# Optimization experiments

Hardware: AMD Instinct MI355X
Metric: run time of the kernel (lower is better)

The kernel has to match this reference:

```python
import jax, jax.numpy as jnp
import numpy as np

PNS = (1, 2, 3, 4, 6, 8, 12, 16)
N_E, E_DIM = 8192, 256
BETA = 0.25
ALPHA = 0.5  # abs(quant_resi)
B, HW = 64, 16


def _area_mat(out_n, in_n):
    # torch adaptive_avg_pool1d matrix (F.interpolate mode='area')
    M = np.zeros((out_n, in_n), np.float32)
    for i in range(out_n):
        s = (i * in_n) // out_n
        e = -((-(i + 1) * in_n) // out_n)  # ceil((i+1)*in_n/out_n)
        M[i, s:e] = 1.0 / (e - s)
    return M


def _cubic_w(t):
    a = -0.75  # torch bicubic coefficient
    t = abs(t)
    if t <= 1.0:
        return (a + 2) * t ** 3 - (a + 3) * t ** 2 + 1.0
    if t < 2.0:
        return a * t ** 3 - 5 * a * t ** 2 + 8 * a * t - 4 * a
    return 0.0


def _bicubic_mat(out_n, in_n):
    # torch F.interpolate mode='bicubic', align_corners=False, border-replicate taps
    M = np.zeros((out_n, in_n), np.float32)
    scale = in_n / out_n
    for i in range(out_n):
        x = (i + 0.5) * scale - 0.5
        f = int(np.floor(x))
        for k in range(-1, 3):
            idx = min(max(f + k, 0), in_n - 1)
            M[i, idx] += _cubic_w(x - (f + k))
    return M


def setup_inputs() -> dict:
    key = jax.random.key(0)
    k1, k2, k3 = jax.random.split(key, 3)
    z = jax.random.normal(k1, (B, E_DIM, HW, HW), jnp.float32)
    embedding = jax.random.normal(k2, (N_E, E_DIM), jnp.float32)
    conv_w = jax.random.normal(k3, (len(PNS), E_DIM, E_DIM, 3, 3), jnp.float32) * 0.02
    conv_b = jnp.zeros((len(PNS), E_DIM), jnp.float32)
    return {"z": z, "embedding": embedding, "conv_w": conv_w, "conv_b": conv_b}


def reference(z, embedding, conv_w, conv_b):
    Bz, C, H, W = z.shape
    S = len(PNS)
    z_rest = z
    z_hat = jnp.zeros_like(z)
    total_loss = jnp.zeros((), z.dtype)
    counts = jnp.zeros((N_E,), z.dtype)
    e_sq = jnp.sum(embedding ** 2, axis=1)  # [n_e]
    for si, pn in enumerate(PNS):
        if si != S - 1:
            A = jnp.asarray(_area_mat(pn, H))
            zd = jnp.einsum('ph,qw,bchw->bpqc', A, A, z_rest)  # [B,pn,pn,C]
        else:
            zd = jnp.transpose(z_rest, (0, 2, 3, 1))
        zf = zd.reshape(-1, C)  # [N,C]
        dist = jnp.sum(zf ** 2, axis=1, keepdims=True) + e_sq - 2.0 * (zf @ embedding.T)
        idx = jnp.argmin(dist, axis=1)  # [N]
        zk = embedding[idx].reshape(zd.shape)  # [B,pn,pn,C]
        zk = jnp.transpose(zk, (0, 3, 1, 2))  # [B,C,pn,pn]
        if si != S - 1:
            U = jnp.asarray(_bicubic_mat(H, pn))
            zu = jnp.einsum('hp,wq,bcpq->bchw', U, U, zk)
        else:
            zu = zk
        y = jax.lax.conv_general_dilated(
            zu, conv_w[si], (1, 1), 'SAME',
            dimension_numbers=('NCHW', 'OIHW', 'NCHW')) + conv_b[si][None, :, None, None]
        res = zu * (1.0 - ALPHA) + y * ALPHA
        z_hat = z_hat + res
        z_rest = z_rest - res
        counts = counts.at[idx].add(jnp.asarray(1.0, z.dtype))
        total_loss = total_loss + BETA * jnp.mean((jax.lax.stop_gradient(z_hat) - z) ** 2)
    mean_vq_loss = total_loss / S
    z_hat_out = z + jax.lax.stop_gradient(z_hat - z)
    return z_hat_out, mean_vq_loss, counts
```

## Files before the change

kernel.cpp:

```cpp
#include <hip/hip_runtime.h>
#include <math.h>

#define NB 64
#define NC 256
#define NHW 16
#define NE 8192
#define NUMEL 4194304
#define LOSS_OFF 4194304
#define CNT_OFF  4194305

typedef __bf16 bf16x8 __attribute__((ext_vector_type(8)));
typedef float  f32x4  __attribute__((ext_vector_type(4)));

#define GLOAD_LDS(gptr, lptr) \
  __builtin_amdgcn_global_load_lds( \
      (const __attribute__((address_space(1))) unsigned int*)(gptr), \
      (__attribute__((address_space(3))) unsigned int*)(lptr), 16, 0, 0)

__device__ __forceinline__ float cubicw(float t) {
  t = fabsf(t);
  if (t <= 1.0f) return (1.25f * t - 2.25f) * t * t + 1.0f;
  if (t < 2.0f)  return ((-0.75f * t + 3.75f) * t - 6.0f) * t + 3.0f;
  return 0.0f;
}

__device__ __forceinline__ short f2bf(float x) {
  union { float f; unsigned int u; } v; v.f = x;
  unsigned int r = v.u + 0x7fffu + ((v.u >> 16) & 1u);
  return (short)(r >> 16);
}
__device__ __forceinline__ float bf2f(short h) {
  union { float f; unsigned int u; } v;
  v.u = ((unsigned int)(unsigned short)h) << 16;
  return v.f;
}

__global__ void k_zero(float* a, int na) {
  int i = blockIdx.x * 256 + threadIdx.x;
  if (i < na) a[i] = 0.0f;
}

__global__ void k_tr_in(const float* __restrict__ z, float* __restrict__ zrest) {
  int n = blockIdx.x, c = threadIdx.x;
  int b = n >> 8, hw = n & 255;
  zrest[(size_t)n * 256 + c] = z[((size_t)(b * 256 + c)) * 256 + hw];
}

__global__ void k_prep_emb2(const float* __restrict__ emb, short* __restrict__ B2,
                            float* __restrict__ esq) {
  int j = blockIdx.x, t = threadIdx.x;
  float v = emb[(size_t)j * 256 + t];
  short hi = f2bf(v);
  short lo = f2bf(v - bf2f(hi));
  B2[(size_t)j * 768 + t]       = hi;
  B2[(size_t)j * 768 + 256 + t] = hi;
  B2[(size_t)j * 768 + 512 + t] = lo;
  __shared__ float red[256];
  red[t] = v * v;
  __syncthreads();
  for (int s = 128; s > 0; s >>= 1) { if (t < s) red[t] += red[t + s]; __syncthreads(); }
  if (t == 0) esq[j] = red[0];
}

__global__ void k_prep_wb(const float* __restrict__ w, short* __restrict__ wB2) {
  int m = blockIdx.x * 256 + threadIdx.x;
  if (m >= 8 * 9 * 65536) return;
  int i = m & 255, o = (m >> 8) & 255;
  int r = m >> 16;
  int si = r / 9, tap = r % 9;
  float v = w[(((size_t)si * 256 + o) * 256 + i) * 9 + tap];
  short hi = f2bf(v);
  short lo = f2bf(v - bf2f(hi));
  size_t dst = ((size_t)r * 256 + o) * 768;
  wB2[dst + i]       = hi;
  wB2[dst + 256 + i] = hi;
  wB2[dst + 512 + i] = lo;
}

__global__ void k_down_a2(const float* __restrict__ zrest, short* __restrict__ A2, int pn) {
  int pq = blockIdx.x, b = blockIdx.y, c = threadIdx.x;
  int p = pq / pn, q = pq % pn;
  int sp = (p * 16) / pn, ep = ((p + 1) * 16 + pn - 1) / pn;
  int sq = (q * 16) / pn, eq = ((q + 1) * 16 + pn - 1) / pn;
  float s = 0.0f;
  for (int h = sp; h < ep; h++)
    for (int w = sq; w < eq; w++)
      s += zrest[((size_t)((b * 16 + h) * 16 + w)) * 256 + c];
  float x = s / (float)((ep - sp) * (eq - sq));
  int n = (b * pn + p) * pn + q;
  short hi = f2bf(x);
  short lo = f2bf(x - bf2f(hi));
  A2[(size_t)n * 768 + c]       = hi;
  A2[(size_t)n * 768 + 256 + c] = lo;
  A2[(size_t)n * 768 + 512 + c] = hi;
}

__global__ void k_split_a2(const float* __restrict__ zrest, short* __restrict__ A2) {
  int n = blockIdx.x, c = threadIdx.x;
  float x = zrest[(size_t)n * 256 + c];
  short hi = f2bf(x);
  short lo = f2bf(x - bf2f(hi));
  A2[(size_t)n * 768 + c]       = hi;
  A2[(size_t)n * 768 + 256 + c] = lo;
  A2[(size_t)n * 768 + 512 + c] = hi;
}

__global__ __launch_bounds__(512, 2) void k_dist_mfma(
    const short* __restrict__ A2, const short* __restrict__ B2,
    const float* __restrict__ esq, float* __restrict__ pd, int* __restrict__ pi,
    int N) {
  __shared__ short As[4][8192];
  __shared__ short Bs[4][8192];
  int t = threadIdx.x, ln = t & 63, wv = t >> 6;
  int wr = wv >> 2, wc = wv & 3;
  int n0 = blockIdx.x * 256;
  int jb0 = blockIdx.y * 256;
  int lc = ln & 15, lq = ln >> 4;

  const short* gA[2]; const short* gB[2]; int ldst[2];
#pragma unroll
  for (int i = 0; i < 2; i++) {
    int C = i * 512 + wv * 64 + ln;
    int L = C >> 3, c5s = C & 7;
    int c5g = c5s ^ (L & 7);
    int rowg = (L << 1) | (c5g >> 2), ccg = c5g & 3;
    gA[i] = A2 + (size_t)(n0 + rowg) * 768 + ccg * 8;
    gB[i] = B2 + (size_t)(jb0 + rowg) * 768 + ccg * 8;
    ldst[i] = (i * 512 + wv * 64) * 8;
  }
  int offA[2][4], offB[4];
#pragma unroll
  for (int rt = 0; rt < 4; rt++) {
#pragma unroll
    for (int h = 0; h < 2; h++) {
      int row = wr * 128 + h * 64 + rt * 16 + lc;
      int L = row >> 1;
      int swc = (((row & 1) << 2) + lq) ^ (L & 7);
      offA[h][rt] = L * 64 + swc * 8;
    }
    int rowb = wc * 64 + rt * 16 + lc;
    int Lb = rowb >> 1;
    int swb = (((rowb & 1) << 2) + lq) ^ (Lb & 7);
    offB[rt] = Lb * 64 + swb * 8;
  }

  f32x4 acc[8][4];
#pragma unroll
  for (int at = 0; at < 8; at++)
#pragma unroll
    for (int ac = 0; ac < 4; ac++) acc[at][ac] = (f32x4)(0.0f);

#define DSTAGE_A(tile_, bsel_)                                        \
  {                                                                   \
    _Pragma("unroll")                                                 \
    for (int i = 0; i < 2; i++)                                       \
      GLOAD_LDS(gA[i] + (tile_) * 32, &As[(bsel_)][ldst[i]]);         \
  }
#define DSTAGE_B(tile_, bsel_)                                        \
  {                                                                   \
    _Pragma("unroll")                                                 \
    for (int i = 0; i < 2; i++)                                       \
      GLOAD_LDS(gB[i] + (tile_) * 32, &Bs[(bsel_)][ldst[i]]);         \
  }

  DSTAGE_A(0, 0); DSTAGE_B(0, 0);
  DSTAGE_A(1, 1); DSTAGE_B(1, 1);
  DSTAGE_A(2, 2); DSTAGE_B(2, 2);
  asm volatile("s_waitcnt vmcnt(8)" ::: "memory");
  __builtin_amdgcn_s_barrier();

#pragma unroll
  for (int kt = 0; kt < 24; kt++) {
    const int bsel = kt & 3;
    const short* aBase = &As[bsel][0];
    const short* bBase = &Bs[bsel][0];
    if (kt < 21) DSTAGE_A(kt + 3, (kt + 3) & 3);
    bf16x8 fa0[4], fb[4];
#pragma unroll
    for (int rt = 0; rt < 4; rt++)
      fa0[rt] = *(const bf16x8*)(aBase + offA[0][rt]);
#pragma unroll
    for (int ct = 0; ct < 4; ct++)
      fb[ct] = *(const bf16x8*)(bBase + offB[ct]);
    __builtin_amdgcn_s_barrier();
    asm volatile("s_waitcnt lgkmcnt(0)" ::: "memory");
    __builtin_amdgcn_s_setprio(1);
#pragma unroll
    for (int rt = 0; rt < 4; rt++)
#pragma unroll
      for (int ct = 0; ct < 4; ct++)
        acc[rt][ct] = __builtin_amdgcn_mfma_f32_16x16x32_bf16(
            fa0[rt], fb[ct], acc[rt][ct], 0, 0, 0);
    __builtin_amdgcn_s_setprio(0);
    __builtin_amdgcn_s_barrier();
    if (kt < 21) DSTAGE_B(kt + 3, (kt + 3) & 3);
    bf16x8 fa1[4];
#pragma unroll
    for (int rt = 0; rt < 4; rt++)
      fa1[rt] = *(const bf16x8*)(aBase + offA[1][rt]);
    __builtin_amdgcn_s_barrier();
    asm volatile("s_waitcnt lgkmcnt(0)" ::: "memory");
    __builtin_amdgcn_s_setprio(1);
#pragma unroll
    for (int rt = 0; rt < 4; rt++)
#pragma unroll
      for (int ct = 0; ct < 4; ct++)
        acc[4 + rt][ct] = __builtin_amdgcn_mfma_f32_16x16x32_bf16(
            fa1[rt], fb[ct], acc[4 + rt][ct], 0, 0, 0);
    __builtin_amdgcn_s_setprio(0);
    if (kt < 23) {
      if (kt < 21)       { asm volatile("s_waitcnt vmcnt(8)" ::: "memory"); }
      else if (kt == 21) { asm volatile("s_waitcnt vmcnt(4)" ::: "memory"); }
      else               { asm volatile("s_waitcnt vmcnt(0)" ::: "memory"); }
      __builtin_amdgcn_s_barrier();
    }
  }
#undef DSTAGE_A
#undef DSTAGE_B

  float* sbd = (float*)(&As[0][0]);
  int*   sbi = (int*)((char*)(&As[0][0]) + 4096);

#pragma unroll
  for (int at = 0; at < 8; at++) {
    float bst[4]; int bix[4];
#pragma unroll
    for (int r = 0; r < 4; r++) { bst[r] = 3.4e38f; bix[r] = 0; }
#pragma unroll
    for (int ac = 0; ac < 4; ac++) {
      int j = jb0 + wc * 64 + ac * 16 + lc;
      float es = esq[j];
#pragma unroll
      for (int r = 0; r < 4; r++) {
        float d = es - 2.0f * acc[at][ac][r];
        if (d < bst[r]) { bst[r] = d; bix[r] = j; }
      }
    }
#pragma unroll
    for (int r = 0; r < 4; r++) {
      float bd = bst[r]; int bi = bix[r];
#pragma unroll
      for (int off = 1; off < 16; off <<= 1) {
        float od = __shfl_xor(bd, off, 64);
        int   oi = __shfl_xor(bi, off, 64);
        if (od < bd || (od == bd && oi < bi)) { bd = od; bi = oi; }
      }
      if (lc == 0) {
        int rl = wr * 128 + at * 16 + lq * 4 + r;
        sbd[wc * 256 + rl] = bd;
        sbi[wc * 256 + rl] = bi;
      }
    }
  }
  __syncthreads();
  if (t < 256) {
    float b0 = sbd[t]; int i0 = sbi[t];
#pragma unroll
    for (int w = 1; w < 4; w++) {
      float b1 = sbd[w * 256 + t]; int i1 = sbi[w * 256 + t];
      if (b1 < b0 || (b1 == b0 && i1 < i0)) { b0 = b1; i0 = i1; }
    }
    int n = n0 + t;
    if (n < N) {
      pd[(size_t)n * 32 + blockIdx.y] = b0;
      pi[(size_t)n * 32 + blockIdx.y] = i0;
    }
  }
}

__global__ void k_red(const float* __restrict__ pd, const int* __restrict__ pi,
                      int* __restrict__ idxb, float* __restrict__ counts, int N, int nct) {
  int n = blockIdx.x * 256 + threadIdx.x;
  if (n >= N) return;
  float bd = pd[(size_t)n * nct]; int bi = pi[(size_t)n * nct];
  for (int jt = 1; jt < nct; jt++) {
    float d = pd[(size_t)n * nct + jt]; int ii = pi[(size_t)n * nct + jt];
    if (d < bd || (d == bd && ii < bi)) { bd = d; bi = ii; }
  }
  idxb[n] = bi;
  atomicAdd(counts + bi, 1.0f);
}

__global__ void k_up(const float* __restrict__ emb, const int* __restrict__ idxb,
                     float* __restrict__ zu, short* __restrict__ zu2, int pn, int last) {
  int n = blockIdx.x, c = threadIdx.x;
  float acc;
  if (last) {
    acc = emb[(size_t)idxb[n] * 256 + c];
  } else {
    int b = n >> 8, hw = n & 255, h = hw >> 4, w = hw & 15;
    float scale = pn / 16.0f;
    float xh = (h + 0.5f) * scale - 0.5f; int fh = (int)floorf(xh);
    float xw = (w + 0.5f) * scale - 0.5f; int fw = (int)floorf(xw);
    int ph[4], pw[4]; float wh[4], wwt[4];
#pragma unroll
    for (int k = 0; k < 4; k++) {
      wh[k] = cubicw(xh - (float)(fh + k - 1));
      int pp = fh + k - 1; ph[k] = min(max(pp, 0), pn - 1);
      wwt[k] = cubicw(xw - (float)(fw + k - 1));
      pp = fw + k - 1; pw[k] = min(max(pp, 0), pn - 1);
    }
    acc = 0.0f;
#pragma unroll
    for (int kh = 0; kh < 4; kh++)
#pragma unroll
      for (int kw = 0; kw < 4; kw++) {
        int row = idxb[(n >> 8) * pn * pn + ph[kh] * pn + pw[kw]];
        acc += wh[kh] * wwt[kw] * emb[(size_t)row * 256 + c];
      }
  }
  zu[(size_t)n * 256 + c] = acc;
  short hi = f2bf(acc);
  short lo = f2bf(acc - bf2f(hi));
  zu2[(size_t)n * 768 + c]       = hi;
  zu2[(size_t)n * 768 + 256 + c] = lo;
  zu2[(size_t)n * 768 + 512 + c] = hi;
}

__global__ __launch_bounds__(256, 2) void k_conv_mfma(
    const short* __restrict__ zu2, const short* __restrict__ wB2,
    const float* __restrict__ cb, const float* __restrict__ zu,
    float* __restrict__ zrest, float* __restrict__ out_loss, int si) {
  __shared__ short Ah[2][108 * 64];
  __shared__ short Bs[3][128 * 64];
  __shared__ float red[256];
  int t = threadIdx.x, ln = t & 63, wv = t >> 6;
  int pxh = wv >> 1, oq = wv & 1;
  int lc = ln & 15, lq = ln >> 4;
  int b = blockIdx.x >> 2, h0 = (blockIdx.x & 3) * 4;
  int o0 = blockIdx.y * 128;

  bool awr[4], aval[4]; const short* asrc[4]; int adst[4];
#pragma unroll
  for (int i = 0; i < 4; i++) {
    int c = i * 256 + t;
    int rh = c >> 3, cc = c & 7;
    int hh = rh / 18, wx = rh - hh * 18;
    int h = h0 + hh - 1, w = wx - 1;
    awr[i]  = (c < 864);
    aval[i] = awr[i] && (h >= 0) && (h < 16) && (w >= 0) && (w < 16);
    int n = aval[i] ? (b * 256 + h * 16 + w) : 0;
    asrc[i] = zu2 + (size_t)n * 768 + cc * 8;
    adst[i] = rh * 64 + (cc ^ (rh & 7)) * 8;
  }

#define CSTAGE(nt_, nk_, bsel_)                                             \
  {                                                                         \
    const short* bbase =                                                    \
        wB2 + (((size_t)si * 9 + (nt_)) * 256 + o0) * 768 + (nk_) * 64;     \
    _Pragma("unroll")                                                       \
    for (int i = 0; i < 4; i++) {                                           \
      int Lb = i * 256 + wv * 64;                                           \
      int L = Lb + ln;                                                      \
      int row = L >> 3, cc = L & 7;                                         \
      int gc = cc ^ (row & 7);                                              \
      GLOAD_LDS(bbase + (size_t)row * 768 + gc * 8, &Bs[(bsel_)][Lb * 8]);  \
    }                                                                       \
  }

  f32x4 acc[2][4];
#pragma unroll
  for (int pf = 0; pf < 2; pf++)
#pragma unroll
    for (int ct = 0; ct < 4; ct++) acc[pf][ct] = (f32x4)(0.0f);

  {
    uint4 a[4];
#pragma unroll
    for (int i = 0; i < 4; i++) {
      a[i] = make_uint4(0u, 0u, 0u, 0u);
      if (aval[i]) a[i] = *(const uint4*)(asrc[i]);
    }
    CSTAGE(0, 0, 0);
    CSTAGE(1, 0, 1);
    asm volatile("s_waitcnt vmcnt(8)" ::: "memory");
#pragma unroll
    for (int i = 0; i < 4; i++)
      if (awr[i]) *(uint4*)(&Ah[0][adst[i]]) = a[i];
    asm volatile("s_waitcnt vmcnt(4) lgkmcnt(0)" ::: "memory");
  }
  __builtin_amdgcn_s_barrier();

  for (int kc = 0; kc < 12; kc++) {
    int ab = kc & 1;
    uint4 na[4];
#pragma unroll
    for (int i = 0; i < 4; i++) na[i] = make_uint4(0u, 0u, 0u, 0u);
#pragma unroll
    for (int tap = 0; tap < 9; tap++) {
      const int rb3 = tap % 3;
      const int sb3 = (tap + 2) % 3;
      int dh = tap / 3 - 1, dw = tap % 3 - 1;
      bf16x8 fa[2][2], fb[2][4];
#pragma unroll
      for (int ks = 0; ks < 2; ks++) {
#pragma unroll
        for (int pf = 0; pf < 2; pf++) {
          int rh = (pxh * 2 + pf + dh + 1) * 18 + lc + dw + 1;
          int cc = (ks * 4 + lq) ^ (rh & 7);
          fa[ks][pf] = *(const bf16x8*)(&Ah[ab][rh * 64 + cc * 8]);
        }
#pragma unroll
        for (int ct = 0; ct < 4; ct++) {
          int row = oq * 64 + ct * 16 + lc;
          int cc = (ks * 4 + lq) ^ (lc & 7);
          fb[ks][ct] = *(const bf16x8*)(&Bs[rb3][row * 64 + cc * 8]);
        }
      }
      if (kc < 11 || tap < 7) {
        int nt = (tap < 7) ? tap + 2 : tap - 7;
        int nk = (tap < 7) ? kc : kc + 1;
        CSTAGE(nt, nk, sb3);
      }
      if (tap == 0 && kc < 11) {
        int koff = (kc + 1) * 64;
#pragma unroll
        for (int i = 0; i < 4; i++)
          if (aval[i]) na[i] = *(const uint4*)(asrc[i] + koff);
      }
      if (tap == 8 && kc < 11) {
#pragma unroll
        for (int i = 0; i < 4; i++)
          if (awr[i]) *(uint4*)(&Ah[ab ^ 1][adst[i]]) = na[i];
      }
      __builtin_amdgcn_s_barrier();
      asm volatile("s_waitcnt lgkmcnt(0)" ::: "memory");
      __builtin_amdgcn_s_setprio(1);
#pragma unroll
      for (int ks = 0; ks < 2; ks++)
#pragma unroll
        for (int pf = 0; pf < 2; pf++)
#pragma unroll
          for (int ct = 0; ct < 4; ct++)
            acc[pf][ct] = __builtin_amdgcn_mfma_f32_16x16x32_bf16(
                fa[ks][pf], fb[ks][ct], acc[pf][ct], 0, 0, 0);
      __builtin_amdgcn_s_setprio(0);
      if (tap <= 1) {
        if (kc < 11) { asm volatile("s_waitcnt vmcnt(8)" ::: "memory"); }
        else         { asm volatile("s_waitcnt vmcnt(4)" ::: "memory"); }
        __builtin_amdgcn_s_barrier();
      } else if (tap <= 6) {
        asm volatile("s_waitcnt vmcnt(4)" ::: "memory");
        __builtin_amdgcn_s_barrier();
      } else if (tap == 7) {
        if (kc < 11) { asm volatile("s_waitcnt vmcnt(4)" ::: "memory"); }
        else         { asm volatile("s_waitcnt vmcnt(0)" ::: "memory"); }
        __builtin_amdgcn_s_barrier();
      } else {
        if (kc < 11) {
          asm volatile("s_waitcnt vmcnt(4) lgkmcnt(0)" ::: "memory");
          __builtin_amdgcn_s_barrier();
        }
      }
    }
  }
#undef CSTAGE
  __syncthreads();

  float lsum = 0.0f;
#pragma unroll
  for (int ct = 0; ct < 4; ct++) {
    int o = o0 + oq * 64 + ct * 16 + lc;
    float bias = cb[si * 256 + o];
#pragma unroll
    for (int pf = 0; pf < 2; pf++) {
      int n = b * 256 + (h0 + pxh * 2 + pf) * 16;
#pragma unroll
      for (int r = 0; r < 4; r++) {
        size_t m = (size_t)(n + lq * 4 + r) * 256 + o;
        float y = acc[pf][ct][r] + bias;
        float res = 0.5f * (zu[m] + y);
        float nv = zrest[m] - res;
        zrest[m] = nv;
        lsum += nv * nv;
      }
    }
  }
  red[t] = lsum;
  __syncthreads();
  for (int s = 128; s > 0; s >>= 1) { if (t < s) red[t] += red[t + s]; __syncthreads(); }
  if (t == 0) atomicAdd(out_loss, red[0] * (0.25f / (8.0f * 4194304.0f)));
}

__global__ void k_out(const float* __restrict__ z, const float* __restrict__ zrest,
                      float* __restrict__ out) {
  int n = blockIdx.x, c = threadIdx.x;
  int b = n >> 8, hw = n & 255;
  size_t m = ((size_t)(b * 256 + c)) * 256 + hw;
  out[m] = z[m] - zrest[(size_t)n * 256 + c];
}

extern "C" void kernel_launch(void* const* d_in, const int* in_sizes, int n_in,
                              void* d_out, int out_size, void* d_ws, size_t ws_size,
                              hipStream_t stream) {
  const float* z   = (const float*)d_in[0];
  const float* emb = (const float*)d_in[1];
  const float* cw  = (const float*)d_in[2];
  const float* cb  = (const float*)d_in[3];
  float* out = (float*)d_out;
  float* ws  = (float*)d_ws;

  float* z_rest = ws;
  float* zu     = ws + 4194304;
  float* esq    = ws + 8388608;
  short* A2     = (short*)(ws + 8396800);
  short* zu2    = A2;
  short* B2     = (short*)(ws + 14688256);
  short* wB2    = (short*)(ws + 17833984);
  float* pd     = ws + 24911872;
  int*   pi     = (int*)(ws + 25436160);
  int*   idxb   = (int*)(ws + 25960448);

  const int pns[8] = {1, 2, 3, 4, 6, 8, 12, 16};

  k_zero<<<33, 256, 0, stream>>>(out + LOSS_OFF, 1 + NE);
  k_tr_in<<<16384, 256, 0, stream>>>(z, z_rest);
  k_prep_emb2<<<8192, 256, 0, stream>>>(emb, B2, esq);
  k_prep_wb<<<18432, 256, 0, stream>>>(cw, wB2);

  for (int si = 0; si < 8; si++) {
    int pn = pns[si];
    int N = 64 * pn * pn;
    if (si < 7)
      k_down_a2<<<dim3(pn * pn, 64), 256, 0, stream>>>(z_rest, A2, pn);
    else
      k_split_a2<<<16384, 256, 0, stream>>>(z_rest, A2);
    int rb = (N + 255) / 256;
    k_dist_mfma<<<dim3(rb, 32), 512, 0, stream>>>(A2, B2, esq, pd, pi, N);
    k_red<<<(N + 255) / 256, 256, 0, stream>>>(pd, pi, idxb, out + CNT_OFF, N, 32);
    k_up<<<16384, 256, 0, stream>>>(emb, idxb, zu, zu2, pn, si == 7 ? 1 : 0);
    k_conv_mfma<<<dim3(256, 2), 256, 0, stream>>>(zu2, wB2, cb, zu, z_rest,
                                                  out + LOSS_OFF, si);
  }
  k_out<<<16384, 256, 0, stream>>>(z, z_rest, out);
}
```

Before: 1.895 ms.

## Restructure conv MFMA to split hi/lo operands separately and tile 2 rows × 256 outputs

```diff
diff --git a/kernel.cpp b/kernel.cpp
--- a/kernel.cpp
+++ b/kernel.cpp
@@ -71,10 +71,9 @@
   float v = w[(((size_t)si * 256 + o) * 256 + i) * 9 + tap];
   short hi = f2bf(v);
   short lo = f2bf(v - bf2f(hi));
-  size_t dst = ((size_t)r * 256 + o) * 768;
+  size_t dst = ((size_t)r * 256 + o) * 512;
   wB2[dst + i]       = hi;
-  wB2[dst + 256 + i] = hi;
-  wB2[dst + 512 + i] = lo;
+  wB2[dst + 256 + i] = lo;
 }
 
 __global__ void k_down_a2(const float* __restrict__ zrest, short* __restrict__ A2, int pn) {
@@ -312,50 +311,62 @@
   zu[(size_t)n * 256 + c] = acc;
   short hi = f2bf(acc);
   short lo = f2bf(acc - bf2f(hi));
-  zu2[(size_t)n * 768 + c]       = hi;
-  zu2[(size_t)n * 768 + 256 + c] = lo;
-  zu2[(size_t)n * 768 + 512 + c] = hi;
+  zu2[(size_t)n * 512 + c]       = hi;
+  zu2[(size_t)n * 512 + 256 + c] = lo;
 }
 
 __global__ __launch_bounds__(256, 2) void k_conv_mfma(
     const short* __restrict__ zu2, const short* __restrict__ wB2,
     const float* __restrict__ cb, const float* __restrict__ zu,
     float* __restrict__ zrest, float* __restrict__ out_loss, int si) {
-  __shared__ short Ah[2][108 * 64];
-  __shared__ short Bs[3][128 * 64];
+  __shared__ short Ah[72 * 64];
+  __shared__ short Bs[2][2][8192];
   __shared__ float red[256];
   int t = threadIdx.x, ln = t & 63, wv = t >> 6;
-  int pxh = wv >> 1, oq = wv & 1;
   int lc = ln & 15, lq = ln >> 4;
-  int b = blockIdx.x >> 2, h0 = (blockIdx.x & 3) * 4;
-  int o0 = blockIdx.y * 128;
-
-  bool awr[4], aval[4]; const short* asrc[4]; int adst[4];
+  int b = blockIdx.x >> 3, r0 = (blockIdx.x & 7) * 2;
+
+  bool hen[3], hval[3]; const short* hsrc[3]; int hdst[3];
+#pragma unroll
+  for (int i = 0; i < 3; i++) {
+    int l = i * 256 + t;
+    hen[i] = (l < 576);
+    int hrow = l >> 3, c3 = l & 7;
+    int part = c3 >> 2, cc = c3 & 3;
+    int hh = hrow / 18, wx = hrow - hh * 18;
+    int h = r0 + hh - 1, w = wx - 1;
+    hval[i] = hen[i] && h >= 0 && h < 16 && w >= 0 && w < 16;
+    int n = hval[i] ? (b * 256 + h * 16 + w) : 0;
+    hsrc[i] = zu2 + (size_t)n * 512 + part * 256 + cc * 8;
+    hdst[i] = (hrow * 8 + (c3 ^ (hrow & 7))) * 8;
+  }
+  const short* gB[4]; int bdst[4];
 #pragma unroll
   for (int i = 0; i < 4; i++) {
-    int c = i * 256 + t;
-    int rh = c >> 3, cc = c & 7;
-    int hh = rh / 18, wx = rh - hh * 18;
-    int h = h0 + hh - 1, w = wx - 1;
-    awr[i]  = (c < 864);
-    aval[i] = awr[i] && (h >= 0) && (h < 16) && (w >= 0) && (w < 16);
-    int n = aval[i] ? (b * 256 + h * 16 + w) : 0;
-    asrc[i] = zu2 + (size_t)n * 768 + cc * 8;
-    adst[i] = rh * 64 + (cc ^ (rh & 7)) * 8;
-  }
-
-#define CSTAGE(nt_, nk_, bsel_)                                             \
+    int C = i * 256 + t;
+    int L = C >> 3, c5s = C & 7;
+    int c5g = c5s ^ (L & 7);
+    int row = (L << 1) | (c5g >> 2), cc = c5g & 3;
+    gB[i] = wB2 + ((size_t)si * 9 * 256 + row) * 512 + cc * 8;
+    bdst[i] = C * 8;
+  }
+  int offB[4];
+#pragma unroll
+  for (int ct = 0; ct < 4; ct++) {
+    int row = wv * 64 + ct * 16 + lc;
+    int L = row >> 1;
+    int swc = (((row & 1) << 2) | lq) ^ (L & 7);
+    offB[ct] = L * 64 + swc * 8;
+  }
+
+#define CSTAGE(tap_, kc_, buf_)                                             \
   {                                                                         \
-    const short* bbase =                                                    \
-        wB2 + (((size_t)si * 9 + (nt_)) * 256 + o0) * 768 + (nk_) * 64;     \
     _Pragma("unroll")                                                       \
-    for (int i = 0; i < 4; i++) {                                           \
-      int Lb = i * 256 + wv * 64;                                           \
-      int L = Lb + ln;                                                      \
-      int row = L >> 3, cc = L & 7;                                         \
-      int gc = cc ^ (row & 7);                                              \
-      GLOAD_LDS(bbase + (size_t)row * 768 + gc * 8, &Bs[(bsel_)][Lb * 8]);  \
-    }                                                                       \
+    for (int p = 0; p < 2; p++)                                             \
+      _Pragma("unroll")                                                     \
+      for (int i = 0; i < 4; i++)                                           \
+        GLOAD_LDS(gB[i] + (size_t)(tap_) * 131072 + p * 256 + (kc_) * 32,   \
+                  &Bs[(buf_)][p][bdst[i]]);                                 \
   }
 
   f32x4 acc[2][4];
@@ -365,92 +376,84 @@
     for (int ct = 0; ct < 4; ct++) acc[pf][ct] = (f32x4)(0.0f);
 
   {
-    uint4 a[4];
-#pragma unroll
-    for (int i = 0; i < 4; i++) {
-      a[i] = make_uint4(0u, 0u, 0u, 0u);
-      if (aval[i]) a[i] = *(const uint4*)(asrc[i]);
+    uint4 hv[3];
+#pragma unroll
+    for (int i = 0; i < 3; i++) {
+      hv[i] = make_uint4(0u, 0u, 0u, 0u);
+      if (hval[i]) hv[i] = *(const uint4*)(hsrc[i]);
     }
     CSTAGE(0, 0, 0);
-    CSTAGE(1, 0, 1);
     asm volatile("s_waitcnt vmcnt(8)" ::: "memory");
 #pragma unroll
-    for (int i = 0; i < 4; i++)
-      if (awr[i]) *(uint4*)(&Ah[0][adst[i]]) = a[i];
-    asm volatile("s_waitcnt vmcnt(4) lgkmcnt(0)" ::: "memory");
+    for (int i = 0; i < 3; i++)
+      if (hen[i]) *(uint4*)(&Ah[hdst[i]]) = hv[i];
+    asm volatile("s_waitcnt vmcnt(0) lgkmcnt(0)" ::: "memory");
   }
   __builtin_amdgcn_s_barrier();
 
-  for (int kc = 0; kc < 12; kc++) {
-    int ab = kc & 1;
-    uint4 na[4];
-#pragma unroll
-    for (int i = 0; i < 4; i++) na[i] = make_uint4(0u, 0u, 0u, 0u);
+  for (int kc = 0; kc < 8; kc++) {
+    uint4 nh[3];
+#pragma unroll
+    for (int i = 0; i < 3; i++) nh[i] = make_uint4(0u, 0u, 0u, 0u);
 #pragma unroll
     for (int tap = 0; tap < 9; tap++) {
-      const int rb3 = tap % 3;
-      const int sb3 = (tap + 2) % 3;
-      int dh = tap / 3 - 1, dw = tap % 3 - 1;
-      bf16x8 fa[2][2], fb[2][4];
-#pragma unroll
-      for (int ks = 0; ks < 2; ks++) {
-#pragma unroll
-        for (int pf = 0; pf < 2; pf++) {
-          int rh = (pxh * 2 + pf + dh + 1) * 18 + lc + dw + 1;
-          int cc = (ks * 4 + lq) ^ (rh & 7);
-          fa[ks][pf] = *(const bf16x8*)(&Ah[ab][rh * 64 + cc * 8]);
-        }
-#pragma unroll
-        for (int ct = 0; ct < 4; ct++) {
-          int row = oq * 64 + ct * 16 + lc;
-          int cc = (ks * 4 + lq) ^ (lc & 7);
-          fb[ks][ct] = *(const bf16x8*)(&Bs[rb3][row * 64 + cc * 8]);
-        }
-      }
-      if (kc < 11 || tap < 7) {
-        int nt = (tap < 7) ? tap + 2 : tap - 7;
-        int nk = (tap < 7) ? kc : kc + 1;
-        CSTAGE(nt, nk, sb3);
-      }
-      if (tap == 0 && kc < 11) {
-        int koff = (kc + 1) * 64;
-#pragma unroll
-        for (int i = 0; i < 4; i++)
-          if (aval[i]) na[i] = *(const uint4*)(asrc[i] + koff);
-      }
-      if (tap == 8 && kc < 11) {
-#pragma unroll
-        for (int i = 0; i < 4; i++)
-          if (awr[i]) *(uint4*)(&Ah[ab ^ 1][adst[i]]) = na[i];
+      const int s = kc * 9 + tap;
+      const int buf = s & 1;
+      const int dh = tap / 3 - 1, dw = tap % 3 - 1;
+      bf16x8 fahi[2], falo[2], fbhi[4], fblo[4];
+#pragma unroll
+      for (int pf = 0; pf < 2; pf++) {
+        int hrow = (pf + dh + 1) * 18 + lc + dw + 1;
+        int base = hrow * 64, sw = hrow & 7;
+        fahi[pf] = *(const bf16x8*)(Ah + base + (lq ^ sw) * 8);
+        falo[pf] = *(const bf16x8*)(Ah + base + ((4 + lq) ^ sw) * 8);
+      }
+#pragma unroll
+      for (int ct = 0; ct < 4; ct++) {
+        fbhi[ct] = *(const bf16x8*)(&Bs[buf][0][offB[ct]]);
+        fblo[ct] = *(const bf16x8*)(&Bs[buf][1][offB[ct]]);
+      }
+      if (s < 71) {
+        int nt = (tap < 8) ? tap + 1 : 0;
+        int nk = (tap < 8) ? kc : kc + 1;
+        CSTAGE(nt, nk, buf ^ 1);
+      }
+      if (tap == 0 && kc < 7) {
+#pragma unroll
+        for (int i = 0; i < 3; i++)
+          if (hval[i]) nh[i] = *(const uint4*)(hsrc[i] + (kc + 1) * 32);
       }
       __builtin_amdgcn_s_barrier();
       asm volatile("s_waitcnt lgkmcnt(0)" ::: "memory");
       __builtin_amdgcn_s_setprio(1);
 #pragma unroll
-      for (int ks = 0; ks < 2; ks++)
-#pragma unroll
-        for (int pf = 0; pf < 2; pf++)
-#pragma unroll
-          for (int ct = 0; ct < 4; ct++)
-            acc[pf][ct] = __builtin_amdgcn_mfma_f32_16x16x32_bf16(
-                fa[ks][pf], fb[ks][ct], acc[pf][ct], 0, 0, 0);
+      for (int pf = 0; pf < 2; pf++)
+#pragma unroll
+        for (int ct = 0; ct < 4; ct++)
+          acc[pf][ct] = __builtin_amdgcn_mfma_f32_16x16x32_bf16(
+              fahi[pf], fbhi[ct], acc[pf][ct], 0, 0, 0);
+#pragma unroll
+      for (int pf = 0; pf < 2; pf++)
+#pragma unroll
+        for (int ct = 0; ct < 4; ct++)
+          acc[pf][ct] = __builtin_amdgcn_mfma_f32_16x16x32_bf16(
+              falo[pf], fbhi[ct], acc[pf][ct], 0, 0, 0);
+#pragma unroll
+      for (int pf = 0; pf < 2; pf++)
+#pragma unroll
+        for (int ct = 0; ct < 4; ct++)
+          acc[pf][ct] = __builtin_amdgcn_mfma_f32_16x16x32_bf16(
+              fahi[pf], fblo[ct], acc[pf][ct], 0, 0, 0);
       __builtin_amdgcn_s_setprio(0);
-      if (tap <= 1) {
-        if (kc < 11) { asm volatile("s_waitcnt vmcnt(8)" ::: "memory"); }
-        else         { asm volatile("s_waitcnt vmcnt(4)" ::: "memory"); }
+      if (tap == 8 && kc < 7) {
         __builtin_amdgcn_s_barrier();
-      } else if (tap <= 6) {
-        asm volatile("s_waitcnt vmcnt(4)" ::: "memory");
+#pragma unroll
+        for (int i = 0; i < 3; i++)
+          if (hen[i]) *(uint4*)(&Ah[hdst[i]]) = nh[i];
+      }
+      if (s < 71) {
+        asm volatile("s_waitcnt vmcnt(0) lgkmcnt(0)" ::: "memory");
         __builtin_amdgcn_s_barrier();
-      } else if (tap == 7) {
-        if (kc < 11) { asm volatile("s_waitcnt vmcnt(4)" ::: "memory"); }
-        else         { asm volatile("s_waitcnt vmcnt(0)" ::: "memory"); }
-        __builtin_amdgcn_s_barrier();
-      } else {
-        if (kc < 11) {
-          asm volatile("s_waitcnt vmcnt(4) lgkmcnt(0)" ::: "memory");
-          __builtin_amdgcn_s_barrier();
-        }
       }
     }
   }
@@ -460,14 +463,15 @@
   float lsum = 0.0f;
 #pragma unroll
   for (int ct = 0; ct < 4; ct++) {
-    int o = o0 + oq * 64 + ct * 16 + lc;
+    int o = wv * 64 + ct * 16 + lc;
     float bias = cb[si * 256 + o];
 #pragma unroll
     for (int pf = 0; pf < 2; pf++) {
-      int n = b * 256 + (h0 + pxh * 2 + pf) * 16;
 #pragma unroll
       for (int r = 0; r < 4; r++) {
-        size_t m = (size_t)(n + lq * 4 + r) * 256 + o;
+        int px = pf * 16 + lq * 4 + r;
+        int n = b * 256 + (r0 + (px >> 4)) * 16 + (px & 15);
+        size_t m = (size_t)n * 256 + o;
         float y = acc[pf][ct][r] + bias;
         float res = 0.5f * (zu[m] + y);
         float nv = zrest[m] - res;
@@ -529,8 +533,8 @@
     k_dist_mfma<<<dim3(rb, 32), 512, 0, stream>>>(A2, B2, esq, pd, pi, N);
     k_red<<<(N + 255) / 256, 256, 0, stream>>>(pd, pi, idxb, out + CNT_OFF, N, 32);
     k_up<<<16384, 256, 0, stream>>>(emb, idxb, zu, zu2, pn, si == 7 ? 1 : 0);
-    k_conv_mfma<<<dim3(256, 2), 256, 0, stream>>>(zu2, wB2, cb, zu, z_rest,
-                                                  out + LOSS_OFF, si);
+    k_conv_mfma<<<dim3(512), 256, 0, stream>>>(zu2, wB2, cb, zu, z_rest,
+                                               out + LOSS_OFF, si);
   }
   k_out<<<16384, 256, 0, stream>>>(z, z_rest, out);
 }
```

Result: slower. 2.013 ms (+6.2%).

## Deepen conv weight pipeline to four stages and single-buffer the A tile

Applied to the files above, without the earlier changes.

```diff
diff --git a/kernel.cpp b/kernel.cpp
--- a/kernel.cpp
+++ b/kernel.cpp
@@ -321,9 +321,8 @@
     const short* __restrict__ zu2, const short* __restrict__ wB2,
     const float* __restrict__ cb, const float* __restrict__ zu,
     float* __restrict__ zrest, float* __restrict__ out_loss, int si) {
-  __shared__ short Ah[2][108 * 64];
-  __shared__ short Bs[3][128 * 64];
-  __shared__ float red[256];
+  __shared__ short Ah[108 * 64];
+  __shared__ short Bs[4][128 * 64];
   int t = threadIdx.x, ln = t & 63, wv = t >> 6;
   int pxh = wv >> 1, oq = wv & 1;
   int lc = ln & 15, lq = ln >> 4;
@@ -373,23 +372,24 @@
     }
     CSTAGE(0, 0, 0);
     CSTAGE(1, 0, 1);
-    asm volatile("s_waitcnt vmcnt(8)" ::: "memory");
+    CSTAGE(2, 0, 2);
+    asm volatile("s_waitcnt vmcnt(12)" ::: "memory");
 #pragma unroll
     for (int i = 0; i < 4; i++)
-      if (awr[i]) *(uint4*)(&Ah[0][adst[i]]) = a[i];
-    asm volatile("s_waitcnt vmcnt(4) lgkmcnt(0)" ::: "memory");
+      if (awr[i]) *(uint4*)(&Ah[adst[i]]) = a[i];
+    asm volatile("s_waitcnt vmcnt(8) lgkmcnt(0)" ::: "memory");
   }
   __builtin_amdgcn_s_barrier();
 
   for (int kc = 0; kc < 12; kc++) {
-    int ab = kc & 1;
     uint4 na[4];
 #pragma unroll
     for (int i = 0; i < 4; i++) na[i] = make_uint4(0u, 0u, 0u, 0u);
 #pragma unroll
     for (int tap = 0; tap < 9; tap++) {
-      const int rb3 = tap % 3;
-      const int sb3 = (tap + 2) % 3;
+      const int s = kc * 9 + tap;
+      const int rb4 = s & 3;
+      const int sb4 = (s + 3) & 3;
       int dh = tap / 3 - 1, dw = tap % 3 - 1;
       bf16x8 fa[2][2], fb[2][4];
 #pragma unroll
@@ -398,30 +398,25 @@
         for (int pf = 0; pf < 2; pf++) {
           int rh = (pxh * 2 + pf + dh + 1) * 18 + lc + dw + 1;
           int cc = (ks * 4 + lq) ^ (rh & 7);
-          fa[ks][pf] = *(const bf16x8*)(&Ah[ab][rh * 64 + cc * 8]);
+          fa[ks][pf] = *(const bf16x8*)(&Ah[rh * 64 + cc * 8]);
         }
 #pragma unroll
         for (int ct = 0; ct < 4; ct++) {
           int row = oq * 64 + ct * 16 + lc;
           int cc = (ks * 4 + lq) ^ (lc & 7);
-          fb[ks][ct] = *(const bf16x8*)(&Bs[rb3][row * 64 + cc * 8]);
+          fb[ks][ct] = *(const bf16x8*)(&Bs[rb4][row * 64 + cc * 8]);
         }
       }
-      if (kc < 11 || tap < 7) {
-        int nt = (tap < 7) ? tap + 2 : tap - 7;
-        int nk = (tap < 7) ? kc : kc + 1;
-        CSTAGE(nt, nk, sb3);
+      if (s <= 104) {
+        int nt = (tap <= 5) ? tap + 3 : tap - 6;
+        int nk = (tap <= 5) ? kc : kc + 1;
+        CSTAGE(nt, nk, sb4);
       }
       if (tap == 0 && kc < 11) {
         int koff = (kc + 1) * 64;
 #pragma unroll
         for (int i = 0; i < 4; i++)
           if (aval[i]) na[i] = *(const uint4*)(asrc[i] + koff);
-      }
-      if (tap == 8 && kc < 11) {
-#pragma unroll
-        for (int i = 0; i < 4; i++)
-          if (awr[i]) *(uint4*)(&Ah[ab ^ 1][adst[i]]) = na[i];
       }
       __builtin_amdgcn_s_barrier();
       asm volatile("s_waitcnt lgkmcnt(0)" ::: "memory");
@@ -435,28 +430,29 @@
             acc[pf][ct] = __builtin_amdgcn_mfma_f32_16x16x32_bf16(
                 fa[ks][pf], fb[ks][ct], acc[pf][ct], 0, 0, 0);
       __builtin_amdgcn_s_setprio(0);
-      if (tap <= 1) {
-        if (kc < 11) { asm volatile("s_waitcnt vmcnt(8)" ::: "memory"); }
-        else         { asm volatile("s_waitcnt vmcnt(4)" ::: "memory"); }
+      if (tap == 8 && kc < 11) {
         __builtin_amdgcn_s_barrier();
-      } else if (tap <= 6) {
-        asm volatile("s_waitcnt vmcnt(4)" ::: "memory");
+#pragma unroll
+        for (int i = 0; i < 4; i++)
+          if (awr[i]) *(uint4*)(&Ah[adst[i]]) = na[i];
+      }
+      if (s < 107) {
+        if (s <= 104) {
+          if (tap == 8) { asm volatile("s_waitcnt vmcnt(8) lgkmcnt(0)" ::: "memory"); }
+          else          { asm volatile("s_waitcnt vmcnt(8)" ::: "memory"); }
+        } else if (s == 105) {
+          asm volatile("s_waitcnt vmcnt(4)" ::: "memory");
+        } else {
+          asm volatile("s_waitcnt vmcnt(0)" ::: "memory");
+        }
         __builtin_amdgcn_s_barrier();
-      } else if (tap == 7) {
-        if (kc < 11) { asm volatile("s_waitcnt vmcnt(4)" ::: "memory"); }
-        else         { asm volatile("s_waitcnt vmcnt(0)" ::: "memory"); }
-        __builtin_amdgcn_s_barrier();
-      } else {
-        if (kc < 11) {
-          asm volatile("s_waitcnt vmcnt(4) lgkmcnt(0)" ::: "memory");
-          __builtin_amdgcn_s_barrier();
-        }
       }
     }
   }
 #undef CSTAGE
   __syncthreads();
 
+  float* red = (float*)Ah;
   float lsum = 0.0f;
 #pragma unroll
   for (int ct = 0; ct < 4; ct++) {
```

Result: no change. 1.862 ms (-1.7%).
